# Kernel tuning notes

Hardware: AMD Instinct MI355X
Metric: run time of the kernel (lower is better)

## Reference

```python
import jax, jax.numpy as jnp
import numpy as np

ALPHA = 0.2  # LeakyReLU negative slope
MASK_VAL = -1e12


def setup_inputs() -> dict:
    key = jax.random.key(0)
    k1, k2, k3, k4 = jax.random.split(key, 4)
    B, N, F_in, F_out = 16, 1024, 128, 64
    inp = jax.random.normal(k1, (B, N, F_in), dtype=jnp.float32)
    adj = jax.random.randint(k2, (B, N, N), 0, 2, dtype=jnp.int32)
    W = jax.random.normal(k3, (F_in, F_out), dtype=jnp.float32) * (1.414 / np.sqrt(F_in))
    a = jax.random.normal(k4, (2 * F_out, 1), dtype=jnp.float32) * (1.414 / np.sqrt(2 * F_out))
    return {"inp": inp, "adj": adj, "W": W, "a": a}


def reference(inp, adj, W, a):
    # inp: [B, N, F_in], adj: [B, N, N], W: [F_in, F_out], a: [2*F_out, 1]
    F_out = W.shape[1]
    h = jnp.einsum('bnf,fo->bno', inp, W)  # [B, N, F_out]
    # e_ij = LeakyReLU(a1 . h_i + a2 . h_j)  (equivalent to concat-then-matmul)
    a1 = a[:F_out, 0]  # [F_out]
    a2 = a[F_out:, 0]  # [F_out]
    e = jax.nn.leaky_relu(
        (h @ a1)[:, :, None] + (h @ a2)[:, None, :], negative_slope=ALPHA
    )  # [B, N, N]
    scores = jnp.where(adj > 0, e, MASK_VAL)
    attention = jax.nn.softmax(scores, axis=-1)  # [B, N, N]
    # dropout with p=0.0 / eval mode -> identity
    h_prime = jnp.einsum('bij,bjo->bio', attention, h)  # [B, N, F_out]
    return jax.nn.elu(h_prime)  # concat=True
```

## Files before the change

kernel.cpp:

```cpp
#include <hip/hip_runtime.h>
#include <cstdint>

#define BB   16
#define NN   1024
#define FIN  128
#define FOUT 64
#define ALPHA_S 0.2f

typedef float    f32x4 __attribute__((ext_vector_type(4)));
typedef _Float16 half8 __attribute__((ext_vector_type(8)));
typedef _Float16 half4 __attribute__((ext_vector_type(4)));

__global__ __launch_bounds__(256) void k_proj(const float* __restrict__ inp,
                                              const float* __restrict__ W,
                                              const float* __restrict__ a,
                                              _Float16* __restrict__ hT,
                                              float* __restrict__ s1,
                                              float* __restrict__ s2){
  __shared__ float red1[4][16];
  __shared__ float red2[4][16];
  const int t = threadIdx.x;
  const int w = t >> 6, lane = t & 63;
  const int m16 = lane & 15, g = lane >> 4;
  const int i0 = blockIdx.x * 16;
  const int b  = i0 >> 10;
  const int j0 = i0 & 1023;
  const int c0 = w * 16;

  const float* arow = inp + (size_t)(i0 + m16) * FIN;

  f32x4 acc = {0.f, 0.f, 0.f, 0.f};
  #pragma unroll
  for (int kk = 0; kk < 4; ++kk){
    const int kbase = kk * 32 + g * 8;
    float4 av0 = *(const float4*)(arow + kbase);
    float4 av1 = *(const float4*)(arow + kbase + 4);
    const float av[8] = {av0.x, av0.y, av0.z, av0.w, av1.x, av1.y, av1.z, av1.w};
    half8 ah, al;
    #pragma unroll
    for (int j = 0; j < 8; ++j){
      _Float16 h = (_Float16)av[j];
      ah[j] = h;
      al[j] = (_Float16)(av[j] - (float)h);
    }
    half8 bh, bl;
    #pragma unroll
    for (int j = 0; j < 8; ++j){
      float wv = W[(kbase + j) * FOUT + c0 + m16];
      _Float16 h = (_Float16)wv;
      bh[j] = h;
      bl[j] = (_Float16)(wv - (float)h);
    }
    acc = __builtin_amdgcn_mfma_f32_16x16x32_f16(ah, bh, acc, 0, 0, 0);
    acc = __builtin_amdgcn_mfma_f32_16x16x32_f16(ah, bl, acc, 0, 0, 0);
    acc = __builtin_amdgcn_mfma_f32_16x16x32_f16(al, bh, acc, 0, 0, 0);
  }

  const float a1c = a[c0 + m16];
  const float a2c = a[FOUT + c0 + m16];
  f32x4 p1, p2;
  #pragma unroll
  for (int q = 0; q < 4; ++q){ p1[q] = acc[q] * a1c; p2[q] = acc[q] * a2c; }
  #pragma unroll
  for (int off = 1; off < 16; off <<= 1){
    #pragma unroll
    for (int q = 0; q < 4; ++q){
      p1[q] += __shfl_xor(p1[q], off, 64);
      p2[q] += __shfl_xor(p2[q], off, 64);
    }
  }
  if (m16 == 0){
    #pragma unroll
    for (int q = 0; q < 4; ++q){
      red1[w][g * 4 + q] = p1[q];
      red2[w][g * 4 + q] = p2[q];
    }
  }

  half4 hv;
  #pragma unroll
  for (int q = 0; q < 4; ++q) hv[q] = (_Float16)acc[q];
  size_t idx = (size_t)b * 65536 + (size_t)(j0 >> 5) * 2048
             + (size_t)(c0 + m16) * 32 + (size_t)(j0 & 31) + (size_t)g * 4;
  *(half4*)(hT + idx) = hv;

  __syncthreads();
  if (t < 16){
    s1[i0 + t] = red1[0][t] + red1[1][t] + red1[2][t] + red1[3][t];
    s2[i0 + t] = red2[0][t] + red2[1][t] + red2[2][t] + red2[3][t];
  }
}

__global__ __launch_bounds__(256) void k_attn(const int* __restrict__ adj,
                                              const _Float16* __restrict__ hT,
                                              const float* __restrict__ s1,
                                              const float* __restrict__ s2,
                                              float* __restrict__ out){
  __shared__ float s2_s[NN];
  __shared__ float redmax[4][16];
  __shared__ float redl[4][16];
  __shared__ float csum[4][1088];

  const int t = threadIdx.x;
  const int w = t >> 6, lane = t & 63;
  const int m16 = lane & 15, g = lane >> 4;
  const int b  = blockIdx.x >> 6;
  const int i0 = (blockIdx.x & 63) * 16;
  const int jb = w * 256;

  *(float4*)&s2_s[jb + lane * 4] = *(const float4*)(s2 + b * NN + jb + lane * 4);

  const float s1i = s1[b * NN + i0 + m16];

  const int* arow = adj + ((size_t)(b * NN + i0 + m16)) * NN + jb + g * 8;
  int4 A0[8], A1[8];
  #pragma unroll
  for (int kk = 0; kk < 8; ++kk){
    A0[kk] = *(const int4*)(arow + kk * 32);
    A1[kk] = *(const int4*)(arow + kk * 32 + 4);
  }

  unsigned mask_lo = 0u, mask_hi = 0u;
  float mxp = -3.0e38f;
  #pragma unroll
  for (int kk = 0; kk < 8; ++kk){
    float4 sA = *(const float4*)&s2_s[jb + kk * 32 + g * 8];
    float4 sB = *(const float4*)&s2_s[jb + kk * 32 + g * 8 + 4];
    unsigned bits = 0u;
    bits |= (A0[kk].x > 0) ? 1u   : 0u;  mxp = fmaxf(mxp, A0[kk].x > 0 ? sA.x : -3.0e38f);
    bits |= (A0[kk].y > 0) ? 2u   : 0u;  mxp = fmaxf(mxp, A0[kk].y > 0 ? sA.y : -3.0e38f);
    bits |= (A0[kk].z > 0) ? 4u   : 0u;  mxp = fmaxf(mxp, A0[kk].z > 0 ? sA.z : -3.0e38f);
    bits |= (A0[kk].w > 0) ? 8u   : 0u;  mxp = fmaxf(mxp, A0[kk].w > 0 ? sA.w : -3.0e38f);
    bits |= (A1[kk].x > 0) ? 16u  : 0u;  mxp = fmaxf(mxp, A1[kk].x > 0 ? sB.x : -3.0e38f);
    bits |= (A1[kk].y > 0) ? 32u  : 0u;  mxp = fmaxf(mxp, A1[kk].y > 0 ? sB.y : -3.0e38f);
    bits |= (A1[kk].z > 0) ? 64u  : 0u;  mxp = fmaxf(mxp, A1[kk].z > 0 ? sB.z : -3.0e38f);
    bits |= (A1[kk].w > 0) ? 128u : 0u;  mxp = fmaxf(mxp, A1[kk].w > 0 ? sB.w : -3.0e38f);
    if (kk < 4) mask_lo |= bits << (kk * 8);
    else        mask_hi |= bits << ((kk - 4) * 8);
  }

  mxp = fmaxf(mxp, __shfl_xor(mxp, 16, 64));
  mxp = fmaxf(mxp, __shfl_xor(mxp, 32, 64));
  if (g == 0) redmax[w][m16] = mxp;
  __syncthreads();
  float mxg = fmaxf(fmaxf(redmax[0][m16], redmax[1][m16]),
                    fmaxf(redmax[2][m16], redmax[3][m16]));
  const bool empty = (mxg < -1.0e38f);
  const float xm = s1i + mxg;
  const float mrow = fmaxf(xm, ALPHA_S * xm);

  f32x4 acc0 = {0,0,0,0}, acc1 = {0,0,0,0}, acc2 = {0,0,0,0}, acc3 = {0,0,0,0};
  float psum = 0.f;
  const size_t bbase = (size_t)b * 65536 + (size_t)(w * 8) * 2048
                     + (size_t)m16 * 32 + (size_t)g * 8;
  const _Float16* bhp = hT + bbase;

  #pragma unroll
  for (int kk = 0; kk < 8; ++kk){
    float4 sA = *(const float4*)&s2_s[jb + kk * 32 + g * 8];
    float4 sB = *(const float4*)&s2_s[jb + kk * 32 + g * 8 + 4];
    const unsigned bits = (kk < 4) ? (mask_lo >> (kk * 8)) : (mask_hi >> ((kk - 4) * 8));
    const float sv[8] = {sA.x, sA.y, sA.z, sA.w, sB.x, sB.y, sB.z, sB.w};
    half8 af;
    #pragma unroll
    for (int u = 0; u < 8; ++u){
      float x = s1i + sv[u];
      float e = fmaxf(x, ALPHA_S * x);
      float p = __expf(e - mrow);
      p = ((bits >> u) & 1u) ? p : 0.0f;
      p = empty ? 1.0f : p;
      af[u] = (_Float16)p;
      psum += (float)af[u];
    }
    half8 b0 = *(const half8*)(bhp + kk * 2048);
    half8 b1 = *(const half8*)(bhp + kk * 2048 + 512);
    half8 b2 = *(const half8*)(bhp + kk * 2048 + 1024);
    half8 b3 = *(const half8*)(bhp + kk * 2048 + 1536);
    acc0 = __builtin_amdgcn_mfma_f32_16x16x32_f16(af, b0, acc0, 0, 0, 0);
    acc1 = __builtin_amdgcn_mfma_f32_16x16x32_f16(af, b1, acc1, 0, 0, 0);
    acc2 = __builtin_amdgcn_mfma_f32_16x16x32_f16(af, b2, acc2, 0, 0, 0);
    acc3 = __builtin_amdgcn_mfma_f32_16x16x32_f16(af, b3, acc3, 0, 0, 0);
  }

  psum += __shfl_xor(psum, 16, 64);
  psum += __shfl_xor(psum, 32, 64);
  if (g == 0) redl[w][m16] = psum;

  #pragma unroll
  for (int q = 0; q < 4; ++q){
    csum[w][(g * 4 + q) * 68 +  0 + m16] = acc0[q];
    csum[w][(g * 4 + q) * 68 + 16 + m16] = acc1[q];
    csum[w][(g * 4 + q) * 68 + 32 + m16] = acc2[q];
    csum[w][(g * 4 + q) * 68 + 48 + m16] = acc3[q];
  }
  __syncthreads();

  const int r  = t >> 4;
  const int c4 = (t & 15) * 4;
  f32x4 sum = *(const f32x4*)&csum[0][r * 68 + c4];
  sum += *(const f32x4*)&csum[1][r * 68 + c4];
  sum += *(const f32x4*)&csum[2][r * 68 + c4];
  sum += *(const f32x4*)&csum[3][r * 68 + c4];
  const float linv = 1.0f / (redl[0][r] + redl[1][r] + redl[2][r] + redl[3][r]);
  f32x4 o;
  #pragma unroll
  for (int u = 0; u < 4; ++u){
    float v = sum[u] * linv;
    o[u] = v > 0.f ? v : __expf(v) - 1.0f;
  }
  *(f32x4*)(out + ((size_t)(b * NN + i0 + r)) * FOUT + c4) = o;
}

extern "C" void kernel_launch(void* const* d_in, const int* in_sizes, int n_in,
                              void* d_out, int out_size, void* d_ws, size_t ws_size,
                              hipStream_t stream) {
  (void)in_sizes; (void)n_in; (void)out_size; (void)ws_size;
  const float* inp = (const float*)d_in[0];
  const int*   adj = (const int*)d_in[1];
  const float* W   = (const float*)d_in[2];
  const float* a   = (const float*)d_in[3];
  float* outp = (float*)d_out;

  _Float16* hT = (_Float16*)d_ws;
  float* s1 = (float*)(hT + (size_t)BB * 65536);
  float* s2 = s1 + BB * NN;

  k_proj<<<BB * NN / 16, 256, 0, stream>>>(inp, W, a, hT, s1, s2);
  k_attn<<<BB * (NN / 16), 256, 0, stream>>>(adj, hT, s1, s2, outp);
}
```

Baseline: 114.6 us.

## Split attention into per-wave column chunks with flash-style partial combine kernel

The 256-thread attention block, whose four waves synchronised through shared memory, becomes 4096 independent single-wave blocks. Each block computes a local row max, a partial softmax sum and partial output for a 256-column chunk and writes them to workspace. A new combine kernel rescales the four partials with exp(m_k - M) and applies the normalisation and ELU. This removes the block barriers and shared-memory staging and loads adj in two halves to cut register pressure, at the cost of an extra launch and extra global traffic for the partials.

```diff
diff --git a/kernel.cpp b/kernel.cpp
--- a/kernel.cpp
+++ b/kernel.cpp
@@ -91,75 +91,69 @@
   }
 }
 
-__global__ __launch_bounds__(256) void k_attn(const int* __restrict__ adj,
+__global__ __launch_bounds__(64) void k_attn4(const int* __restrict__ adj,
                                               const _Float16* __restrict__ hT,
                                               const float* __restrict__ s1,
                                               const float* __restrict__ s2,
-                                              float* __restrict__ out){
-  __shared__ float s2_s[NN];
-  __shared__ float redmax[4][16];
-  __shared__ float redl[4][16];
-  __shared__ float csum[4][1088];
-
-  const int t = threadIdx.x;
-  const int w = t >> 6, lane = t & 63;
+                                              float* __restrict__ pC,
+                                              float* __restrict__ pML){
+  const int lane = threadIdx.x;
   const int m16 = lane & 15, g = lane >> 4;
-  const int b  = blockIdx.x >> 6;
-  const int i0 = (blockIdx.x & 63) * 16;
-  const int jb = w * 256;
-
-  *(float4*)&s2_s[jb + lane * 4] = *(const float4*)(s2 + b * NN + jb + lane * 4);
+  const int tile = blockIdx.x >> 2, q = blockIdx.x & 3;
+  const int b  = tile >> 6;
+  const int i0 = (tile & 63) * 16;
+  const int jb = q * 256;
 
   const float s1i = s1[b * NN + i0 + m16];
-
+  const float* s2b = s2 + b * NN + jb;
   const int* arow = adj + ((size_t)(b * NN + i0 + m16)) * NN + jb + g * 8;
-  int4 A0[8], A1[8];
-  #pragma unroll
-  for (int kk = 0; kk < 8; ++kk){
-    A0[kk] = *(const int4*)(arow + kk * 32);
-    A1[kk] = *(const int4*)(arow + kk * 32 + 4);
-  }
 
   unsigned mask_lo = 0u, mask_hi = 0u;
   float mxp = -3.0e38f;
   #pragma unroll
-  for (int kk = 0; kk < 8; ++kk){
-    float4 sA = *(const float4*)&s2_s[jb + kk * 32 + g * 8];
-    float4 sB = *(const float4*)&s2_s[jb + kk * 32 + g * 8 + 4];
-    unsigned bits = 0u;
-    bits |= (A0[kk].x > 0) ? 1u   : 0u;  mxp = fmaxf(mxp, A0[kk].x > 0 ? sA.x : -3.0e38f);
-    bits |= (A0[kk].y > 0) ? 2u   : 0u;  mxp = fmaxf(mxp, A0[kk].y > 0 ? sA.y : -3.0e38f);
-    bits |= (A0[kk].z > 0) ? 4u   : 0u;  mxp = fmaxf(mxp, A0[kk].z > 0 ? sA.z : -3.0e38f);
-    bits |= (A0[kk].w > 0) ? 8u   : 0u;  mxp = fmaxf(mxp, A0[kk].w > 0 ? sA.w : -3.0e38f);
-    bits |= (A1[kk].x > 0) ? 16u  : 0u;  mxp = fmaxf(mxp, A1[kk].x > 0 ? sB.x : -3.0e38f);
-    bits |= (A1[kk].y > 0) ? 32u  : 0u;  mxp = fmaxf(mxp, A1[kk].y > 0 ? sB.y : -3.0e38f);
-    bits |= (A1[kk].z > 0) ? 64u  : 0u;  mxp = fmaxf(mxp, A1[kk].z > 0 ? sB.z : -3.0e38f);
-    bits |= (A1[kk].w > 0) ? 128u : 0u;  mxp = fmaxf(mxp, A1[kk].w > 0 ? sB.w : -3.0e38f);
-    if (kk < 4) mask_lo |= bits << (kk * 8);
-    else        mask_hi |= bits << ((kk - 4) * 8);
+  for (int h = 0; h < 2; ++h){
+    int4 A0[4], A1[4];
+    #pragma unroll
+    for (int k = 0; k < 4; ++k){
+      A0[k] = *(const int4*)(arow + (h * 4 + k) * 32);
+      A1[k] = *(const int4*)(arow + (h * 4 + k) * 32 + 4);
+    }
+    unsigned accb = 0u;
+    #pragma unroll
+    for (int k = 0; k < 4; ++k){
+      const int kk = h * 4 + k;
+      float4 sA = *(const float4*)(s2b + kk * 32 + g * 8);
+      float4 sB = *(const float4*)(s2b + kk * 32 + g * 8 + 4);
+      unsigned bits = 0u;
+      bits |= (A0[k].x > 0) ? 1u   : 0u;  mxp = fmaxf(mxp, A0[k].x > 0 ? sA.x : -3.0e38f);
+      bits |= (A0[k].y > 0) ? 2u   : 0u;  mxp = fmaxf(mxp, A0[k].y > 0 ? sA.y : -3.0e38f);
+      bits |= (A0[k].z > 0) ? 4u   : 0u;  mxp = fmaxf(mxp, A0[k].z > 0 ? sA.z : -3.0e38f);
+      bits |= (A0[k].w > 0) ? 8u   : 0u;  mxp = fmaxf(mxp, A0[k].w > 0 ? sA.w : -3.0e38f);
+      bits |= (A1[k].x > 0) ? 16u  : 0u;  mxp = fmaxf(mxp, A1[k].x > 0 ? sB.x : -3.0e38f);
+      bits |= (A1[k].y > 0) ? 32u  : 0u;  mxp = fmaxf(mxp, A1[k].y > 0 ? sB.y : -3.0e38f);
+      bits |= (A1[k].z > 0) ? 64u  : 0u;  mxp = fmaxf(mxp, A1[k].z > 0 ? sB.z : -3.0e38f);
+      bits |= (A1[k].w > 0) ? 128u : 0u;  mxp = fmaxf(mxp, A1[k].w > 0 ? sB.w : -3.0e38f);
+      accb |= bits << (k * 8);
+    }
+    if (h == 0) mask_lo = accb; else mask_hi = accb;
   }
 
   mxp = fmaxf(mxp, __shfl_xor(mxp, 16, 64));
   mxp = fmaxf(mxp, __shfl_xor(mxp, 32, 64));
-  if (g == 0) redmax[w][m16] = mxp;
-  __syncthreads();
-  float mxg = fmaxf(fmaxf(redmax[0][m16], redmax[1][m16]),
-                    fmaxf(redmax[2][m16], redmax[3][m16]));
-  const bool empty = (mxg < -1.0e38f);
-  const float xm = s1i + mxg;
+  const bool empty = (mxp < -1.0e38f);
+  const float xm = s1i + mxp;
   const float mrow = fmaxf(xm, ALPHA_S * xm);
 
   f32x4 acc0 = {0,0,0,0}, acc1 = {0,0,0,0}, acc2 = {0,0,0,0}, acc3 = {0,0,0,0};
   float psum = 0.f;
-  const size_t bbase = (size_t)b * 65536 + (size_t)(w * 8) * 2048
-                     + (size_t)m16 * 32 + (size_t)g * 8;
-  const _Float16* bhp = hT + bbase;
+  const _Float16* bhp = hT + (size_t)b * 65536 + (size_t)(jb >> 5) * 2048
+                      + (size_t)m16 * 32 + (size_t)g * 8;
 
   #pragma unroll
   for (int kk = 0; kk < 8; ++kk){
-    float4 sA = *(const float4*)&s2_s[jb + kk * 32 + g * 8];
-    float4 sB = *(const float4*)&s2_s[jb + kk * 32 + g * 8 + 4];
-    const unsigned bits = (kk < 4) ? (mask_lo >> (kk * 8)) : (mask_hi >> ((kk - 4) * 8));
+    float4 sA = *(const float4*)(s2b + kk * 32 + g * 8);
+    float4 sB = *(const float4*)(s2b + kk * 32 + g * 8 + 4);
+    const unsigned bits = ((kk < 4) ? (mask_lo >> (kk * 8)) : (mask_hi >> ((kk - 4) * 8))) & 0xffu;
     const float sv[8] = {sA.x, sA.y, sA.z, sA.w, sB.x, sB.y, sB.z, sB.w};
     half8 af;
     #pragma unroll
@@ -184,31 +178,53 @@
 
   psum += __shfl_xor(psum, 16, 64);
   psum += __shfl_xor(psum, 32, 64);
-  if (g == 0) redl[w][m16] = psum;
-
-  #pragma unroll
-  for (int q = 0; q < 4; ++q){
-    csum[w][(g * 4 + q) * 68 +  0 + m16] = acc0[q];
-    csum[w][(g * 4 + q) * 68 + 16 + m16] = acc1[q];
-    csum[w][(g * 4 + q) * 68 + 32 + m16] = acc2[q];
-    csum[w][(g * 4 + q) * 68 + 48 + m16] = acc3[q];
-  }
-  __syncthreads();
-
-  const int r  = t >> 4;
-  const int c4 = (t & 15) * 4;
-  f32x4 sum = *(const f32x4*)&csum[0][r * 68 + c4];
-  sum += *(const f32x4*)&csum[1][r * 68 + c4];
-  sum += *(const f32x4*)&csum[2][r * 68 + c4];
-  sum += *(const f32x4*)&csum[3][r * 68 + c4];
-  const float linv = 1.0f / (redl[0][r] + redl[1][r] + redl[2][r] + redl[3][r]);
-  f32x4 o;
-  #pragma unroll
-  for (int u = 0; u < 4; ++u){
-    float v = sum[u] * linv;
-    o[u] = v > 0.f ? v : __expf(v) - 1.0f;
-  }
-  *(f32x4*)(out + ((size_t)(b * NN + i0 + r)) * FOUT + c4) = o;
+
+  float* pc = pC + (size_t)blockIdx.x * 1024;
+  #pragma unroll
+  for (int qr = 0; qr < 4; ++qr){
+    pc[(g * 4 + qr) * 64 +  0 + m16] = acc0[qr];
+    pc[(g * 4 + qr) * 64 + 16 + m16] = acc1[qr];
+    pc[(g * 4 + qr) * 64 + 32 + m16] = acc2[qr];
+    pc[(g * 4 + qr) * 64 + 48 + m16] = acc3[qr];
+  }
+  if (g == 0){
+    pML[(size_t)blockIdx.x * 32 + m16]      = empty ? -3.0e38f : mrow;
+    pML[(size_t)blockIdx.x * 32 + 16 + m16] = psum;
+  }
+}
+
+__global__ __launch_bounds__(64) void k_comb(const float* __restrict__ pC,
+                                             const float* __restrict__ pML,
+                                             float* __restrict__ out){
+  const int c = threadIdx.x;
+  const int tile = blockIdx.x;
+  const int b  = tile >> 6;
+  const int i0 = (tile & 63) * 16;
+  const size_t base = (size_t)tile * 4;
+  const float* ml0 = pML + (base + 0) * 32;
+  const float* ml1 = pML + (base + 1) * 32;
+  const float* ml2 = pML + (base + 2) * 32;
+  const float* ml3 = pML + (base + 3) * 32;
+  const float* c0p = pC + (base + 0) * 1024 + c;
+  const float* c1p = pC + (base + 1) * 1024 + c;
+  const float* c2p = pC + (base + 2) * 1024 + c;
+  const float* c3p = pC + (base + 3) * 1024 + c;
+
+  #pragma unroll 4
+  for (int r = 0; r < 16; ++r){
+    float m0 = ml0[r], m1 = ml1[r], m2 = ml2[r], m3 = ml3[r];
+    float l0 = ml0[16 + r], l1 = ml1[16 + r], l2 = ml2[16 + r], l3 = ml3[16 + r];
+    float C0 = c0p[r * 64], C1 = c1p[r * 64], C2 = c2p[r * 64], C3 = c3p[r * 64];
+    float M = fmaxf(fmaxf(m0, m1), fmaxf(m2, m3));
+    float w0 = __expf(m0 - M);
+    float w1 = __expf(m1 - M);
+    float w2 = __expf(m2 - M);
+    float w3 = __expf(m3 - M);
+    float den = fmaf(w0, l0, fmaf(w1, l1, fmaf(w2, l2, w3 * l3)));
+    float num = fmaf(w0, C0, fmaf(w1, C1, fmaf(w2, C2, w3 * C3)));
+    float v = num / den;
+    out[((size_t)(b * NN + i0 + r)) * FOUT + c] = v > 0.f ? v : __expf(v) - 1.0f;
+  }
 }
 
 extern "C" void kernel_launch(void* const* d_in, const int* in_sizes, int n_in,
@@ -222,9 +238,12 @@
   float* outp = (float*)d_out;
 
   _Float16* hT = (_Float16*)d_ws;
-  float* s1 = (float*)(hT + (size_t)BB * 65536);
-  float* s2 = s1 + BB * NN;
-
-  k_proj<<<BB * NN / 16, 256, 0, stream>>>(inp, W, a, hT, s1, s2);
-  k_attn<<<BB * (NN / 16), 256, 0, stream>>>(adj, hT, s1, s2, outp);
-}
+  float* s1  = (float*)(hT + (size_t)BB * 65536);
+  float* s2  = s1 + BB * NN;
+  float* pC  = s2 + BB * NN;
+  float* pML = pC + (size_t)4096 * 1024;
+
+  k_proj <<<BB * NN / 16,    256, 0, stream>>>(inp, W, a, hT, s1, s2);
+  k_attn4<<<BB * (NN/16)*4,   64, 0, stream>>>(adj, hT, s1, s2, pC, pML);
+  k_comb <<<BB * (NN/16),     64, 0, stream>>>(pC, pML, outp);
+}
```

After: 125.0 us. +9.1%, slower.

## Coalesce adjacency loads row-wise and build masks via wave ballots

Applied to the files above, without the earlier changes.

Each wave now loads adjacency rows contiguously, one lane per 4 columns across 16 rows, instead of 16 rows scattered by lane. Mask bits come from __ballot, then each lane pulls out the bits for its own row, and per-row masked maxima use a full-wave shuffle reduction. Launch bounds also request 3 waves per SIMD for occupancy. The aim is better coalescing of the dominant adj read, at the cost of more shuffles, 64-bit bit extraction and possible register pressure.

```diff
diff --git a/kernel.cpp b/kernel.cpp
--- a/kernel.cpp
+++ b/kernel.cpp
@@ -10,6 +10,12 @@
 typedef float    f32x4 __attribute__((ext_vector_type(4)));
 typedef _Float16 half8 __attribute__((ext_vector_type(8)));
 typedef _Float16 half4 __attribute__((ext_vector_type(4)));
+
+__device__ inline float wave_max(float v){
+  #pragma unroll
+  for (int off = 32; off; off >>= 1) v = fmaxf(v, __shfl_xor(v, off, 64));
+  return v;
+}
 
 __global__ __launch_bounds__(256) void k_proj(const float* __restrict__ inp,
                                               const float* __restrict__ W,
@@ -91,11 +97,11 @@
   }
 }
 
-__global__ __launch_bounds__(256) void k_attn(const int* __restrict__ adj,
-                                              const _Float16* __restrict__ hT,
-                                              const float* __restrict__ s1,
-                                              const float* __restrict__ s2,
-                                              float* __restrict__ out){
+__global__ __launch_bounds__(256, 3) void k_attn(const int* __restrict__ adj,
+                                                 const _Float16* __restrict__ hT,
+                                                 const float* __restrict__ s1,
+                                                 const float* __restrict__ s2,
+                                                 float* __restrict__ out){
   __shared__ float s2_s[NN];
   __shared__ float redmax[4][16];
   __shared__ float redl[4][16];
@@ -108,40 +114,40 @@
   const int i0 = (blockIdx.x & 63) * 16;
   const int jb = w * 256;
 
-  *(float4*)&s2_s[jb + lane * 4] = *(const float4*)(s2 + b * NN + jb + lane * 4);
+  float4 s2own = *(const float4*)(s2 + b * NN + jb + lane * 4);
+  *(float4*)&s2_s[jb + lane * 4] = s2own;
 
   const float s1i = s1[b * NN + i0 + m16];
 
-  const int* arow = adj + ((size_t)(b * NN + i0 + m16)) * NN + jb + g * 8;
-  int4 A0[8], A1[8];
-  #pragma unroll
-  for (int kk = 0; kk < 8; ++kk){
-    A0[kk] = *(const int4*)(arow + kk * 32);
-    A1[kk] = *(const int4*)(arow + kk * 32 + 4);
-  }
-
-  unsigned mask_lo = 0u, mask_hi = 0u;
-  float mxp = -3.0e38f;
-  #pragma unroll
-  for (int kk = 0; kk < 8; ++kk){
-    float4 sA = *(const float4*)&s2_s[jb + kk * 32 + g * 8];
-    float4 sB = *(const float4*)&s2_s[jb + kk * 32 + g * 8 + 4];
-    unsigned bits = 0u;
-    bits |= (A0[kk].x > 0) ? 1u   : 0u;  mxp = fmaxf(mxp, A0[kk].x > 0 ? sA.x : -3.0e38f);
-    bits |= (A0[kk].y > 0) ? 2u   : 0u;  mxp = fmaxf(mxp, A0[kk].y > 0 ? sA.y : -3.0e38f);
-    bits |= (A0[kk].z > 0) ? 4u   : 0u;  mxp = fmaxf(mxp, A0[kk].z > 0 ? sA.z : -3.0e38f);
-    bits |= (A0[kk].w > 0) ? 8u   : 0u;  mxp = fmaxf(mxp, A0[kk].w > 0 ? sA.w : -3.0e38f);
-    bits |= (A1[kk].x > 0) ? 16u  : 0u;  mxp = fmaxf(mxp, A1[kk].x > 0 ? sB.x : -3.0e38f);
-    bits |= (A1[kk].y > 0) ? 32u  : 0u;  mxp = fmaxf(mxp, A1[kk].y > 0 ? sB.y : -3.0e38f);
-    bits |= (A1[kk].z > 0) ? 64u  : 0u;  mxp = fmaxf(mxp, A1[kk].z > 0 ? sB.z : -3.0e38f);
-    bits |= (A1[kk].w > 0) ? 128u : 0u;  mxp = fmaxf(mxp, A1[kk].w > 0 ? sB.w : -3.0e38f);
-    if (kk < 4) mask_lo |= bits << (kk * 8);
-    else        mask_hi |= bits << ((kk - 4) * 8);
-  }
-
-  mxp = fmaxf(mxp, __shfl_xor(mxp, 16, 64));
-  mxp = fmaxf(mxp, __shfl_xor(mxp, 32, 64));
-  if (g == 0) redmax[w][m16] = mxp;
+  const int* abase = adj + ((size_t)(b * NN + i0)) * NN + jb + lane * 4;
+  int4 A[16];
+  #pragma unroll
+  for (int r = 0; r < 16; ++r) A[r] = *(const int4*)(abase + (size_t)r * NN);
+
+  unsigned long long bal0 = 0, bal1 = 0, bal2 = 0, bal3 = 0;
+  float rowmax_mine = -3.0e38f;
+  #pragma unroll
+  for (int r = 0; r < 16; ++r){
+    const int4 a4 = A[r];
+    unsigned long long c0 = __ballot(a4.x > 0);
+    unsigned long long c1 = __ballot(a4.y > 0);
+    unsigned long long c2 = __ballot(a4.z > 0);
+    unsigned long long c3 = __ballot(a4.w > 0);
+    float mm = -3.0e38f;
+    mm = fmaxf(mm, a4.x > 0 ? s2own.x : -3.0e38f);
+    mm = fmaxf(mm, a4.y > 0 ? s2own.y : -3.0e38f);
+    mm = fmaxf(mm, a4.z > 0 ? s2own.z : -3.0e38f);
+    mm = fmaxf(mm, a4.w > 0 ? s2own.w : -3.0e38f);
+    mm = wave_max(mm);
+    const bool mine = (r == m16);
+    bal0 = mine ? c0 : bal0;
+    bal1 = mine ? c1 : bal1;
+    bal2 = mine ? c2 : bal2;
+    bal3 = mine ? c3 : bal3;
+    rowmax_mine = mine ? mm : rowmax_mine;
+  }
+
+  if (g == 0) redmax[w][m16] = rowmax_mine;
   __syncthreads();
   float mxg = fmaxf(fmaxf(redmax[0][m16], redmax[1][m16]),
                     fmaxf(redmax[2][m16], redmax[3][m16]));
@@ -151,15 +157,23 @@
 
   f32x4 acc0 = {0,0,0,0}, acc1 = {0,0,0,0}, acc2 = {0,0,0,0}, acc3 = {0,0,0,0};
   float psum = 0.f;
-  const size_t bbase = (size_t)b * 65536 + (size_t)(w * 8) * 2048
-                     + (size_t)m16 * 32 + (size_t)g * 8;
-  const _Float16* bhp = hT + bbase;
+  const _Float16* bhp = hT + (size_t)b * 65536 + (size_t)(jb >> 5) * 2048
+                      + (size_t)m16 * 32 + (size_t)g * 8;
 
   #pragma unroll
   for (int kk = 0; kk < 8; ++kk){
     float4 sA = *(const float4*)&s2_s[jb + kk * 32 + g * 8];
     float4 sB = *(const float4*)&s2_s[jb + kk * 32 + g * 8 + 4];
-    const unsigned bits = (kk < 4) ? (mask_lo >> (kk * 8)) : (mask_hi >> ((kk - 4) * 8));
+    const int sh = kk * 8 + g * 2;
+    const unsigned bits8 =
+        ((unsigned)(bal0 >> sh)       & 1u)        |
+       (((unsigned)(bal1 >> sh)       & 1u) << 1)  |
+       (((unsigned)(bal2 >> sh)       & 1u) << 2)  |
+       (((unsigned)(bal3 >> sh)       & 1u) << 3)  |
+       (((unsigned)(bal0 >> (sh + 1)) & 1u) << 4)  |
+       (((unsigned)(bal1 >> (sh + 1)) & 1u) << 5)  |
+       (((unsigned)(bal2 >> (sh + 1)) & 1u) << 6)  |
+       (((unsigned)(bal3 >> (sh + 1)) & 1u) << 7);
     const float sv[8] = {sA.x, sA.y, sA.z, sA.w, sB.x, sB.y, sB.z, sB.w};
     half8 af;
     #pragma unroll
@@ -167,7 +181,7 @@
       float x = s1i + sv[u];
       float e = fmaxf(x, ALPHA_S * x);
       float p = __expf(e - mrow);
-      p = ((bits >> u) & 1u) ? p : 0.0f;
+      p = ((bits8 >> u) & 1u) ? p : 0.0f;
       p = empty ? 1.0f : p;
       af[u] = (_Float16)p;
       psum += (float)af[u];
```

Result: slower. 117.5 us (+2.6%).

## Pack adjacency into bitmask in projection kernel, read bits in attention

Applied to the files above, without the earlier changes.

The projection kernel now also reads the int32 adjacency rows and packs them with wave ballots into a 1-bit-per-edge mask, which it writes to workspace. The attention kernel then loads 128 bytes of mask per row instead of the full 4 KB of int32 adjacency. The intent is to move the adjacency streaming into the first kernel, where it can overlap with the projection work, and to shrink the attention kernel's load and register footprint. The full 64 MB adjacency read still happens, so total traffic is unchanged or slightly higher, and the projection kernel becomes heavier.

```diff
diff --git a/kernel.cpp b/kernel.cpp
--- a/kernel.cpp
+++ b/kernel.cpp
@@ -14,9 +14,11 @@
 __global__ __launch_bounds__(256) void k_proj(const float* __restrict__ inp,
                                               const float* __restrict__ W,
                                               const float* __restrict__ a,
+                                              const int* __restrict__ adj,
                                               _Float16* __restrict__ hT,
                                               float* __restrict__ s1,
-                                              float* __restrict__ s2){
+                                              float* __restrict__ s2,
+                                              uint32_t* __restrict__ mask){
   __shared__ float red1[4][16];
   __shared__ float red2[4][16];
   const int t = threadIdx.x;
@@ -27,14 +29,29 @@
   const int j0 = i0 & 1023;
   const int c0 = w * 16;
 
-  const float* arow = inp + (size_t)(i0 + m16) * FIN;
+  #pragma unroll
+  for (int q = 0; q < 4; ++q){
+    const int grow = i0 + w * 4 + q;
+    const int* arow = adj + (size_t)grow * NN;
+    uint32_t myword = 0u;
+    #pragma unroll
+    for (int c = 0; c < 16; ++c){
+      int v = arow[c * 64 + lane];
+      unsigned long long bal = __ballot(v > 0);
+      uint32_t half = (lane & 1) ? (uint32_t)(bal >> 32) : (uint32_t)bal;
+      myword = ((lane >> 1) == c) ? half : myword;
+    }
+    if (lane < 32) mask[(size_t)grow * 32 + lane] = myword;
+  }
+
+  const float* arowf = inp + (size_t)(i0 + m16) * FIN;
 
   f32x4 acc = {0.f, 0.f, 0.f, 0.f};
   #pragma unroll
   for (int kk = 0; kk < 4; ++kk){
     const int kbase = kk * 32 + g * 8;
-    float4 av0 = *(const float4*)(arow + kbase);
-    float4 av1 = *(const float4*)(arow + kbase + 4);
+    float4 av0 = *(const float4*)(arowf + kbase);
+    float4 av1 = *(const float4*)(arowf + kbase + 4);
     const float av[8] = {av0.x, av0.y, av0.z, av0.w, av1.x, av1.y, av1.z, av1.w};
     half8 ah, al;
     #pragma unroll
@@ -91,7 +108,7 @@
   }
 }
 
-__global__ __launch_bounds__(256) void k_attn(const int* __restrict__ adj,
+__global__ __launch_bounds__(256) void k_attn(const uint32_t* __restrict__ mask,
                                               const _Float16* __restrict__ hT,
                                               const float* __restrict__ s1,
                                               const float* __restrict__ s2,
@@ -112,33 +129,22 @@
 
   const float s1i = s1[b * NN + i0 + m16];
 
-  const int* arow = adj + ((size_t)(b * NN + i0 + m16)) * NN + jb + g * 8;
-  int4 A0[8], A1[8];
-  #pragma unroll
-  for (int kk = 0; kk < 8; ++kk){
-    A0[kk] = *(const int4*)(arow + kk * 32);
-    A1[kk] = *(const int4*)(arow + kk * 32 + 4);
-  }
-
-  unsigned mask_lo = 0u, mask_hi = 0u;
+  const uint32_t* mrow = mask + ((size_t)(b * NN + i0 + m16)) * 32 + w * 8;
+  const uint4 mwa = *(const uint4*)mrow;
+  const uint4 mwb = *(const uint4*)(mrow + 4);
+  const uint32_t mw[8] = {mwa.x, mwa.y, mwa.z, mwa.w, mwb.x, mwb.y, mwb.z, mwb.w};
+
   float mxp = -3.0e38f;
   #pragma unroll
   for (int kk = 0; kk < 8; ++kk){
     float4 sA = *(const float4*)&s2_s[jb + kk * 32 + g * 8];
     float4 sB = *(const float4*)&s2_s[jb + kk * 32 + g * 8 + 4];
-    unsigned bits = 0u;
-    bits |= (A0[kk].x > 0) ? 1u   : 0u;  mxp = fmaxf(mxp, A0[kk].x > 0 ? sA.x : -3.0e38f);
-    bits |= (A0[kk].y > 0) ? 2u   : 0u;  mxp = fmaxf(mxp, A0[kk].y > 0 ? sA.y : -3.0e38f);
-    bits |= (A0[kk].z > 0) ? 4u   : 0u;  mxp = fmaxf(mxp, A0[kk].z > 0 ? sA.z : -3.0e38f);
-    bits |= (A0[kk].w > 0) ? 8u   : 0u;  mxp = fmaxf(mxp, A0[kk].w > 0 ? sA.w : -3.0e38f);
-    bits |= (A1[kk].x > 0) ? 16u  : 0u;  mxp = fmaxf(mxp, A1[kk].x > 0 ? sB.x : -3.0e38f);
-    bits |= (A1[kk].y > 0) ? 32u  : 0u;  mxp = fmaxf(mxp, A1[kk].y > 0 ? sB.y : -3.0e38f);
-    bits |= (A1[kk].z > 0) ? 64u  : 0u;  mxp = fmaxf(mxp, A1[kk].z > 0 ? sB.z : -3.0e38f);
-    bits |= (A1[kk].w > 0) ? 128u : 0u;  mxp = fmaxf(mxp, A1[kk].w > 0 ? sB.w : -3.0e38f);
-    if (kk < 4) mask_lo |= bits << (kk * 8);
-    else        mask_hi |= bits << ((kk - 4) * 8);
-  }
-
+    const uint32_t bits8 = (mw[kk] >> (g * 8)) & 0xffu;
+    const float sv[8] = {sA.x, sA.y, sA.z, sA.w, sB.x, sB.y, sB.z, sB.w};
+    #pragma unroll
+    for (int u = 0; u < 8; ++u)
+      mxp = fmaxf(mxp, ((bits8 >> u) & 1u) ? sv[u] : -3.0e38f);
+  }
   mxp = fmaxf(mxp, __shfl_xor(mxp, 16, 64));
   mxp = fmaxf(mxp, __shfl_xor(mxp, 32, 64));
   if (g == 0) redmax[w][m16] = mxp;
@@ -147,27 +153,26 @@
                     fmaxf(redmax[2][m16], redmax[3][m16]));
   const bool empty = (mxg < -1.0e38f);
   const float xm = s1i + mxg;
-  const float mrow = fmaxf(xm, ALPHA_S * xm);
+  const float mrowmax = fmaxf(xm, ALPHA_S * xm);
 
   f32x4 acc0 = {0,0,0,0}, acc1 = {0,0,0,0}, acc2 = {0,0,0,0}, acc3 = {0,0,0,0};
   float psum = 0.f;
-  const size_t bbase = (size_t)b * 65536 + (size_t)(w * 8) * 2048
-                     + (size_t)m16 * 32 + (size_t)g * 8;
-  const _Float16* bhp = hT + bbase;
+  const _Float16* bhp = hT + (size_t)b * 65536 + (size_t)(jb >> 5) * 2048
+                      + (size_t)m16 * 32 + (size_t)g * 8;
 
   #pragma unroll
   for (int kk = 0; kk < 8; ++kk){
     float4 sA = *(const float4*)&s2_s[jb + kk * 32 + g * 8];
     float4 sB = *(const float4*)&s2_s[jb + kk * 32 + g * 8 + 4];
-    const unsigned bits = (kk < 4) ? (mask_lo >> (kk * 8)) : (mask_hi >> ((kk - 4) * 8));
+    const uint32_t bits8 = (mw[kk] >> (g * 8)) & 0xffu;
     const float sv[8] = {sA.x, sA.y, sA.z, sA.w, sB.x, sB.y, sB.z, sB.w};
     half8 af;
     #pragma unroll
     for (int u = 0; u < 8; ++u){
       float x = s1i + sv[u];
       float e = fmaxf(x, ALPHA_S * x);
-      float p = __expf(e - mrow);
-      p = ((bits >> u) & 1u) ? p : 0.0f;
+      float p = __expf(e - mrowmax);
+      p = ((bits8 >> u) & 1u) ? p : 0.0f;
       p = empty ? 1.0f : p;
       af[u] = (_Float16)p;
       psum += (float)af[u];
@@ -221,10 +226,11 @@
   const float* a   = (const float*)d_in[3];
   float* outp = (float*)d_out;
 
-  _Float16* hT = (_Float16*)d_ws;
-  float* s1 = (float*)(hT + (size_t)BB * 65536);
-  float* s2 = s1 + BB * NN;
-
-  k_proj<<<BB * NN / 16, 256, 0, stream>>>(inp, W, a, hT, s1, s2);
-  k_attn<<<BB * (NN / 16), 256, 0, stream>>>(adj, hT, s1, s2, outp);
+  _Float16* hT   = (_Float16*)d_ws;
+  float* s1      = (float*)(hT + (size_t)BB * 65536);
+  float* s2      = s1 + BB * NN;
+  uint32_t* mask = (uint32_t*)(s2 + BB * NN);
+
+  k_proj<<<BB * NN / 16, 256, 0, stream>>>(inp, W, a, adj, hT, s1, s2, mask);
+  k_attn<<<BB * (NN / 16), 256, 0, stream>>>(mask, hT, s1, s2, outp);
 }
```

New measurement: 116.8 us. Within noise of the previous version (+2.0%).
